# Performance work log

Hardware: AMD Instinct MI355X
Metric: run time of the kernel (lower is better)

Reference implementation:

```python
import jax, jax.numpy as jnp
import numpy as np

EMBED = 2048
NUM_EXPERTS = 64
TOP_K = 8


def setup_inputs() -> dict:
    key = jax.random.key(0)
    k1, k2, k3 = jax.random.split(key, 3)
    inputs = jax.random.normal(k1, (8, 4096, EMBED), dtype=jnp.float32)
    # nn.Linear(embed_size, num_experts): weight [num_experts, embed_size], bias [num_experts]
    W = jax.random.normal(k2, (NUM_EXPERTS, EMBED), dtype=jnp.float32) / np.sqrt(EMBED)
    b = jax.random.normal(k3, (NUM_EXPERTS,), dtype=jnp.float32) * 0.01
    return {"inputs": inputs, "W": W, "b": b}


def reference(inputs, W, b):
    # Linear projection: [B, S, E] x [E, N] -> [B, S, N]
    logits = jnp.einsum('bse,ne->bsn', inputs, W) + b
    # top-k selection along expert axis
    _, indices = jax.lax.top_k(logits, TOP_K)  # [B, S, K] int32
    # scatter mask: 1 at selected experts (one_hot sum == scatter_ of ones)
    mask = jax.nn.one_hot(indices, NUM_EXPERTS, dtype=jnp.bool_).any(axis=-2)  # [B, S, N]
    # masked_fill(-inf) + softmax -> probs only on selected experts
    masked = jnp.where(mask, logits, -jnp.inf)
    probs = jax.nn.softmax(masked, axis=-1)
    return probs, indices
```

## Files before the change

kernel.cpp:

```cpp
#include <hip/hip_runtime.h>
#include <cmath>

#define NTOK 32768
#define EMB  2048
#define NEXP 64
#define TOPK 8
#define BT   64
#define KC   64

typedef __attribute__((ext_vector_type(4))) double d4;

__global__ __launch_bounds__(256) void router_mfma(
    const float* __restrict__ X,
    const float* __restrict__ W,
    const float* __restrict__ Bv,
    float* __restrict__ out)
{
    __shared__ float xs[BT * KC];
    __shared__ float ws[NEXP * KC];

    const int tid  = threadIdx.x;
    const int lane = tid & 63;
    const int wv   = tid >> 6;
    const int t0   = blockIdx.x * BT;
    const int eL   = lane & 15;
    const int q    = lane >> 4;
    const int sw   = 4 * (eL & 7);

    d4 acc[4];
    #pragma unroll
    for (int c = 0; c < 4; ++c) {
        const double b = (double)Bv[c * 16 + eL];
        acc[c] = (d4){b, b, b, b};
    }

    for (int kc0 = 0; kc0 < EMB; kc0 += KC) {
        #pragma unroll
        for (int j = 0; j < 4; ++j) {
            const int flat = tid + j * 256;
            const int r    = flat >> 4;
            const int a    = flat & 15;
            const float4 vx = *(const float4*)&X[(size_t)(t0 + r) * EMB + kc0 + 4 * a];
            const float4 vw = *(const float4*)&W[(size_t)r * EMB + kc0 + 4 * a];
            const int col = a ^ (r & 7);
            *(float4*)&xs[r * KC + 4 * col] = vx;
            *(float4*)&ws[r * KC + 4 * col] = vw;
        }
        __syncthreads();

        #pragma unroll
        for (int k4 = 0; k4 < KC; k4 += 4) {
            const int kk = (k4 + q) ^ sw;
            const double aF = (double)xs[(wv * 16 + eL) * KC + kk];
            #pragma unroll
            for (int c = 0; c < 4; ++c) {
                const double bF = (double)ws[(c * 16 + eL) * KC + kk];
                acc[c] = __builtin_amdgcn_mfma_f64_16x16x4f64(aF, bF, acc[c], 0, 0, 0);
            }
        }
        __syncthreads();
    }

    float* probs = out;
    float* idxo  = out + (size_t)NTOK * NEXP;

    #pragma unroll
    for (int i = 0; i < 4; ++i) {
        const int T = t0 + wv * 16 + q + 4 * i;
        double v[4];
        #pragma unroll
        for (int c = 0; c < 4; ++c) v[c] = acc[c][i];

        unsigned sel = 0;
        double m0 = 0.0;
        float ssum = 0.0f;
        int myIdx = 0;
        #pragma unroll
        for (int it = 0; it < TOPK; ++it) {
            double bv = -1.0e300;
            int    be = 1 << 30;
            #pragma unroll
            for (int c = 0; c < 4; ++c)
                if (!((sel >> c) & 1) && v[c] > bv) { bv = v[c]; be = c * 16 + eL; }
            double gv = bv; int ge = be;
            #pragma unroll
            for (int off = 1; off <= 8; off <<= 1) {
                const double ov = __shfl_xor(gv, off, 64);
                const int    oe = __shfl_xor(ge, off, 64);
                if (ov > gv || (ov == gv && oe < ge)) { gv = ov; ge = oe; }
            }
            if (it == 0) m0 = gv;
            ssum += __expf((float)(gv - m0));
            if ((ge & 15) == eL) sel |= 1u << (ge >> 4);
            if (eL == it) myIdx = ge;
        }
        const float inv = 1.0f / ssum;
        #pragma unroll
        for (int c = 0; c < 4; ++c) {
            const float p = ((sel >> c) & 1) ? __expf((float)(v[c] - m0)) * inv : 0.0f;
            probs[(size_t)T * NEXP + c * 16 + eL] = p;
        }
        if (eL < TOPK) idxo[(size_t)T * TOPK + eL] = (float)myIdx;
    }
}

extern "C" void kernel_launch(void* const* d_in, const int* in_sizes, int n_in,
                              void* d_out, int out_size, void* d_ws, size_t ws_size,
                              hipStream_t stream) {
    const float* X = (const float*)d_in[0];
    const float* W = (const float*)d_in[1];
    const float* B = (const float*)d_in[2];
    router_mfma<<<NTOK / BT, 256, 0, stream>>>(X, W, B, (float*)d_out);
}
```

Baseline: 456.5 us.

## Double-buffer LDS tiles and prefetch next K-chunk into registers during MFMA

```diff
diff --git a/kernel.cpp b/kernel.cpp
--- a/kernel.cpp
+++ b/kernel.cpp
@@ -7,6 +7,7 @@
 #define TOPK 8
 #define BT   64
 #define KC   64
+#define NCH  (EMB / KC)
 
 typedef __attribute__((ext_vector_type(4))) double d4;
 
@@ -16,8 +17,8 @@
     const float* __restrict__ Bv,
     float* __restrict__ out)
 {
-    __shared__ float xs[BT * KC];
-    __shared__ float ws[NEXP * KC];
+    __shared__ float xs[2][BT * KC];
+    __shared__ float ws[2][NEXP * KC];
 
     const int tid  = threadIdx.x;
     const int lane = tid & 63;
@@ -34,30 +35,53 @@
         acc[c] = (d4){b, b, b, b};
     }
 
-    for (int kc0 = 0; kc0 < EMB; kc0 += KC) {
+    float4 rx[4], rw[4];
+
+    auto load_chunk = [&](int ch) {
+        const int kc0 = ch * KC;
         #pragma unroll
         for (int j = 0; j < 4; ++j) {
             const int flat = tid + j * 256;
             const int r    = flat >> 4;
             const int a    = flat & 15;
-            const float4 vx = *(const float4*)&X[(size_t)(t0 + r) * EMB + kc0 + 4 * a];
-            const float4 vw = *(const float4*)&W[(size_t)r * EMB + kc0 + 4 * a];
-            const int col = a ^ (r & 7);
-            *(float4*)&xs[r * KC + 4 * col] = vx;
-            *(float4*)&ws[r * KC + 4 * col] = vw;
+            rx[j] = *(const float4*)&X[(size_t)(t0 + r) * EMB + kc0 + 4 * a];
+            rw[j] = *(const float4*)&W[(size_t)r * EMB + kc0 + 4 * a];
         }
-        __syncthreads();
+    };
+    auto store_chunk = [&](int buf) {
+        #pragma unroll
+        for (int j = 0; j < 4; ++j) {
+            const int flat = tid + j * 256;
+            const int r    = flat >> 4;
+            const int a    = flat & 15;
+            const int col  = a ^ (r & 7);
+            *(float4*)&xs[buf][r * KC + 4 * col] = rx[j];
+            *(float4*)&ws[buf][r * KC + 4 * col] = rw[j];
+        }
+    };
 
+    load_chunk(0);
+    store_chunk(0);
+    __syncthreads();
+
+    for (int ch = 0; ch < NCH; ++ch) {
+        const int cur = ch & 1;
+        if (ch + 1 < NCH) load_chunk(ch + 1);
+
+        const float* xb = &xs[cur][(wv * 16 + eL) * KC];
+        const float* wb = ws[cur];
         #pragma unroll
         for (int k4 = 0; k4 < KC; k4 += 4) {
             const int kk = (k4 + q) ^ sw;
-            const double aF = (double)xs[(wv * 16 + eL) * KC + kk];
+            const double aF = (double)xb[kk];
             #pragma unroll
             for (int c = 0; c < 4; ++c) {
-                const double bF = (double)ws[(c * 16 + eL) * KC + kk];
+                const double bF = (double)wb[(c * 16 + eL) * KC + kk];
                 acc[c] = __builtin_amdgcn_mfma_f64_16x16x4f64(aF, bF, acc[c], 0, 0, 0);
             }
         }
+
+        if (ch + 1 < NCH) store_chunk((ch + 1) & 1);
         __syncthreads();
     }
 
```

Result: slower. 586.2 us (+28.4%).

## Load GEMM operands directly into registers with double-buffered prefetch, dropping LDS

Applied to the files above, without the earlier changes.

```diff
diff --git a/kernel.cpp b/kernel.cpp
--- a/kernel.cpp
+++ b/kernel.cpp
@@ -6,26 +6,28 @@
 #define NEXP 64
 #define TOPK 8
 #define BT   64
-#define KC   64
+#define KC   16
+#define NCH  (EMB / KC)
 
 typedef __attribute__((ext_vector_type(4))) double d4;
 
-__global__ __launch_bounds__(256) void router_mfma(
+__global__ __launch_bounds__(256, 4) void router_mfma(
     const float* __restrict__ X,
     const float* __restrict__ W,
     const float* __restrict__ Bv,
     float* __restrict__ out)
 {
-    __shared__ float xs[BT * KC];
-    __shared__ float ws[NEXP * KC];
-
     const int tid  = threadIdx.x;
     const int lane = tid & 63;
     const int wv   = tid >> 6;
     const int t0   = blockIdx.x * BT;
     const int eL   = lane & 15;
     const int q    = lane >> 4;
-    const int sw   = 4 * (eL & 7);
+
+    const float* xr = X + (size_t)(t0 + wv * 16 + eL) * EMB + q;
+    const float* wr[4];
+    #pragma unroll
+    for (int c = 0; c < 4; ++c) wr[c] = W + (size_t)(c * 16 + eL) * EMB + q;
 
     d4 acc[4];
     #pragma unroll
@@ -34,32 +36,42 @@
         acc[c] = (d4){b, b, b, b};
     }
 
-    for (int kc0 = 0; kc0 < EMB; kc0 += KC) {
-        #pragma unroll
-        for (int j = 0; j < 4; ++j) {
-            const int flat = tid + j * 256;
-            const int r    = flat >> 4;
-            const int a    = flat & 15;
-            const float4 vx = *(const float4*)&X[(size_t)(t0 + r) * EMB + kc0 + 4 * a];
-            const float4 vw = *(const float4*)&W[(size_t)r * EMB + kc0 + 4 * a];
-            const int col = a ^ (r & 7);
-            *(float4*)&xs[r * KC + 4 * col] = vx;
-            *(float4*)&ws[r * KC + 4 * col] = vw;
-        }
-        __syncthreads();
+    float a0[4], a1[4], b0[16], b1[16];
 
-        #pragma unroll
-        for (int k4 = 0; k4 < KC; k4 += 4) {
-            const int kk = (k4 + q) ^ sw;
-            const double aF = (double)xs[(wv * 16 + eL) * KC + kk];
-            #pragma unroll
-            for (int c = 0; c < 4; ++c) {
-                const double bF = (double)ws[(c * 16 + eL) * KC + kk];
-                acc[c] = __builtin_amdgcn_mfma_f64_16x16x4f64(aF, bF, acc[c], 0, 0, 0);
-            }
-        }
-        __syncthreads();
+#define LOADC(ch, A, B)                                        \
+    {                                                          \
+        const int kc = (ch) * KC;                              \
+        _Pragma("unroll")                                      \
+        for (int s = 0; s < 4; ++s) {                          \
+            A[s] = xr[kc + 4 * s];                             \
+            _Pragma("unroll")                                  \
+            for (int c = 0; c < 4; ++c)                        \
+                B[c * 4 + s] = wr[c][kc + 4 * s];              \
+        }                                                      \
     }
+
+#define COMPUTE(A, B)                                          \
+    {                                                          \
+        _Pragma("unroll")                                      \
+        for (int s = 0; s < 4; ++s) {                          \
+            const double aF = (double)A[s];                    \
+            _Pragma("unroll")                                  \
+            for (int c = 0; c < 4; ++c)                        \
+                acc[c] = __builtin_amdgcn_mfma_f64_16x16x4f64( \
+                    aF, (double)B[c * 4 + s], acc[c], 0, 0, 0);\
+        }                                                      \
+    }
+
+    LOADC(0, a0, b0);
+    LOADC(1, a1, b1);
+    for (int ch = 0; ch < NCH; ch += 2) {
+        COMPUTE(a0, b0);
+        if (ch + 2 < NCH) LOADC(ch + 2, a0, b0);
+        COMPUTE(a1, b1);
+        if (ch + 3 < NCH) LOADC(ch + 3, a1, b1);
+    }
+#undef LOADC
+#undef COMPUTE
 
     float* probs = out;
     float* idxo  = out + (size_t)NTOK * NEXP;
```

Result: slower. 833.6 us (+82.6%).

## Replace FP64 MFMA router GEMM with split-bf16 MFMA plus FP64 refinement of near-ties

Applied to the files above, without the earlier changes.

```diff
diff --git a/kernel.cpp b/kernel.cpp
--- a/kernel.cpp
+++ b/kernel.cpp
@@ -6,101 +6,214 @@
 #define NEXP 64
 #define TOPK 8
 #define BT   64
-#define KC   64
-
-typedef __attribute__((ext_vector_type(4))) double d4;
-
-__global__ __launch_bounds__(256) void router_mfma(
-    const float* __restrict__ X,
-    const float* __restrict__ W,
-    const float* __restrict__ Bv,
-    float* __restrict__ out)
+#define KC   32
+#define NCH  (EMB / KC)
+#define DELTA 1e-4f
+#define WL_CAP 32768
+#define WOFF  (256*1024)
+#define PLANE (NEXP*EMB)
+
+typedef __attribute__((ext_vector_type(8))) short bf8;
+typedef __attribute__((ext_vector_type(4))) float f4;
+
+__device__ __forceinline__ unsigned short bf16rn(float x){
+    union{float f; unsigned u;} c; c.f = x;
+    return (unsigned short)((c.u + 0x7FFFu + ((c.u >> 16) & 1u)) >> 16);
+}
+__device__ __forceinline__ float bf2f(unsigned short b){
+    union{unsigned u; float f;} c; c.u = ((unsigned)b) << 16; return c.f;
+}
+__device__ __forceinline__ void gld16(const void* g, void* lds){
+    __builtin_amdgcn_global_load_lds(
+        (const __attribute__((address_space(1))) void*)g,
+        (__attribute__((address_space(3))) void*)lds, 16, 0, 0);
+}
+
+__global__ __launch_bounds__(256) void wsplit(const float* __restrict__ W,
+                                              unsigned short* __restrict__ wp){
+    int i = blockIdx.x * 256 + threadIdx.x;
+    #pragma unroll
+    for (int rep = 0; rep < 2; ++rep, i += 65536){
+        const float x = W[i];
+        const unsigned short b1 = bf16rn(x);  const float r  = x - bf2f(b1);
+        const unsigned short b2 = bf16rn(r);  const float r2 = r - bf2f(b2);
+        const unsigned short b3 = bf16rn(r2);
+        wp[i] = b1; wp[PLANE + i] = b2; wp[2*PLANE + i] = b3;
+    }
+}
+
+__global__ __launch_bounds__(256) void router_bf16(
+    const float* __restrict__ X, const unsigned short* __restrict__ WP,
+    const float* __restrict__ Bv, float* __restrict__ out, int* __restrict__ wsi)
 {
-    __shared__ float xs[BT * KC];
-    __shared__ float ws[NEXP * KC];
-
-    const int tid  = threadIdx.x;
-    const int lane = tid & 63;
-    const int wv   = tid >> 6;
-    const int t0   = blockIdx.x * BT;
-    const int eL   = lane & 15;
-    const int q    = lane >> 4;
-    const int sw   = 4 * (eL & 7);
-
-    d4 acc[4];
+    __shared__ __align__(16) unsigned short xs[2][3][BT*KC];
+    __shared__ __align__(16) unsigned short wsh[2][3][NEXP*KC];
+
+    const int tid = threadIdx.x, lane = tid & 63, wv = tid >> 6;
+    const int t0 = blockIdx.x * BT;
+    const int eL = lane & 15, q = lane >> 4;
+
+    const int sr = tid >> 2, sj = tid & 3;
+    const float* xg = X + (size_t)(t0 + sr)*EMB + 8*sj;
+    const int rw = wv*16 + (lane >> 2);
+    const unsigned short* wg = WP + (size_t)rw*EMB + 8*(lane & 3);
+
+    f4 acc[4];
     #pragma unroll
-    for (int c = 0; c < 4; ++c) {
-        const double b = (double)Bv[c * 16 + eL];
-        acc[c] = (d4){b, b, b, b};
-    }
-
-    for (int kc0 = 0; kc0 < EMB; kc0 += KC) {
-        #pragma unroll
-        for (int j = 0; j < 4; ++j) {
-            const int flat = tid + j * 256;
-            const int r    = flat >> 4;
-            const int a    = flat & 15;
-            const float4 vx = *(const float4*)&X[(size_t)(t0 + r) * EMB + kc0 + 4 * a];
-            const float4 vw = *(const float4*)&W[(size_t)r * EMB + kc0 + 4 * a];
-            const int col = a ^ (r & 7);
-            *(float4*)&xs[r * KC + 4 * col] = vx;
-            *(float4*)&ws[r * KC + 4 * col] = vw;
-        }
-        __syncthreads();
-
-        #pragma unroll
-        for (int k4 = 0; k4 < KC; k4 += 4) {
-            const int kk = (k4 + q) ^ sw;
-            const double aF = (double)xs[(wv * 16 + eL) * KC + kk];
-            #pragma unroll
-            for (int c = 0; c < 4; ++c) {
-                const double bF = (double)ws[(c * 16 + eL) * KC + kk];
-                acc[c] = __builtin_amdgcn_mfma_f64_16x16x4f64(aF, bF, acc[c], 0, 0, 0);
-            }
-        }
+    for (int c = 0; c < 4; ++c){ const float b = Bv[c*16+eL]; acc[c] = (f4){b,b,b,b}; }
+
+    float xr[8];
+    auto loadX = [&](int ch){
+        const float4 v0 = *(const float4*)(xg + (size_t)ch*KC);
+        const float4 v1 = *(const float4*)(xg + (size_t)ch*KC + 4);
+        xr[0]=v0.x; xr[1]=v0.y; xr[2]=v0.z; xr[3]=v0.w;
+        xr[4]=v1.x; xr[5]=v1.y; xr[6]=v1.z; xr[7]=v1.w;
+    };
+    auto gldW = [&](int ch, int buf){
+        #pragma unroll
+        for (int s = 0; s < 3; ++s)
+            gld16(wg + (size_t)s*PLANE + ch*KC, &wsh[buf][s][wv*512]);
+    };
+    auto writeX = [&](int buf){
+        bf8 o0, o1, o2;
+        #pragma unroll
+        for (int j = 0; j < 8; ++j){
+            const float x = xr[j];
+            const unsigned short b1 = bf16rn(x);  const float r  = x - bf2f(b1);
+            const unsigned short b2 = bf16rn(r);  const float r2 = r - bf2f(b2);
+            o0[j] = (short)b1; o1[j] = (short)b2; o2[j] = (short)bf16rn(r2);
+        }
+        *(bf8*)&xs[buf][0][sr*KC + 8*sj] = o0;
+        *(bf8*)&xs[buf][1][sr*KC + 8*sj] = o1;
+        *(bf8*)&xs[buf][2][sr*KC + 8*sj] = o2;
+    };
+
+    loadX(0); gldW(0, 0); writeX(0);
+    __syncthreads();
+
+    for (int ch = 0; ch < NCH; ++ch){
+        const int buf = ch & 1;
+        if (ch + 1 < NCH){ loadX(ch+1); gldW(ch+1, buf^1); }
+
+        const int rA = (wv*16 + eL)*KC + q*8;
+        const bf8 a0 = *(const bf8*)&xs[buf][0][rA];
+        const bf8 a1 = *(const bf8*)&xs[buf][1][rA];
+        const bf8 a2 = *(const bf8*)&xs[buf][2][rA];
+        #pragma unroll
+        for (int c = 0; c < 4; ++c){
+            const int rB = (c*16 + eL)*KC + q*8;
+            const bf8 b0 = *(const bf8*)&wsh[buf][0][rB];
+            const bf8 b1 = *(const bf8*)&wsh[buf][1][rB];
+            const bf8 b2 = *(const bf8*)&wsh[buf][2][rB];
+            acc[c] = __builtin_amdgcn_mfma_f32_16x16x32_bf16(a1, b1, acc[c], 0,0,0);
+            acc[c] = __builtin_amdgcn_mfma_f32_16x16x32_bf16(a0, b2, acc[c], 0,0,0);
+            acc[c] = __builtin_amdgcn_mfma_f32_16x16x32_bf16(a2, b0, acc[c], 0,0,0);
+            acc[c] = __builtin_amdgcn_mfma_f32_16x16x32_bf16(a0, b1, acc[c], 0,0,0);
+            acc[c] = __builtin_amdgcn_mfma_f32_16x16x32_bf16(a1, b0, acc[c], 0,0,0);
+            acc[c] = __builtin_amdgcn_mfma_f32_16x16x32_bf16(a0, b0, acc[c], 0,0,0);
+        }
+        if (ch + 1 < NCH) writeX(buf^1);
         __syncthreads();
     }
 
     float* probs = out;
     float* idxo  = out + (size_t)NTOK * NEXP;
+    int* wl = wsi + 4;
 
     #pragma unroll
-    for (int i = 0; i < 4; ++i) {
-        const int T = t0 + wv * 16 + q + 4 * i;
-        double v[4];
+    for (int i = 0; i < 4; ++i){
+        const int T = t0 + wv*16 + 4*q + i;
+        float v[4];
         #pragma unroll
         for (int c = 0; c < 4; ++c) v[c] = acc[c][i];
 
-        unsigned sel = 0;
-        double m0 = 0.0;
-        float ssum = 0.0f;
+        unsigned sel = 0; float m0 = 0.0f, ssum = 0.0f, prevm = 0.0f, mingap = 1e30f;
         int myIdx = 0;
         #pragma unroll
-        for (int it = 0; it < TOPK; ++it) {
-            double bv = -1.0e300;
-            int    be = 1 << 30;
+        for (int it = 0; it < 9; ++it){
+            float bv = -1e30f; int be = 1 << 30;
             #pragma unroll
             for (int c = 0; c < 4; ++c)
-                if (!((sel >> c) & 1) && v[c] > bv) { bv = v[c]; be = c * 16 + eL; }
-            double gv = bv; int ge = be;
+                if (!((sel >> c) & 1) && v[c] > bv){ bv = v[c]; be = c*16 + eL; }
+            float gv = bv; int ge = be;
             #pragma unroll
-            for (int off = 1; off <= 8; off <<= 1) {
-                const double ov = __shfl_xor(gv, off, 64);
-                const int    oe = __shfl_xor(ge, off, 64);
-                if (ov > gv || (ov == gv && oe < ge)) { gv = ov; ge = oe; }
+            for (int off = 1; off <= 8; off <<= 1){
+                const float ov = __shfl_xor(gv, off, 64);
+                const int   oe = __shfl_xor(ge, off, 64);
+                if (ov > gv || (ov == gv && oe < ge)){ gv = ov; ge = oe; }
             }
-            if (it == 0) m0 = gv;
-            ssum += __expf((float)(gv - m0));
-            if ((ge & 15) == eL) sel |= 1u << (ge >> 4);
-            if (eL == it) myIdx = ge;
+            if (it > 0) mingap = fminf(mingap, prevm - gv);
+            prevm = gv;
+            if (it < 8){
+                if (it == 0) m0 = gv;
+                ssum += __expf(gv - m0);
+                if ((ge & 15) == eL) sel |= 1u << (ge >> 4);
+                if (eL == it) myIdx = ge;
+            }
+        }
+        if (eL == 0 && mingap < DELTA){
+            const int pos = atomicAdd(wsi, 1);
+            if (pos < WL_CAP) wl[pos] = T;
         }
         const float inv = 1.0f / ssum;
         #pragma unroll
-        for (int c = 0; c < 4; ++c) {
-            const float p = ((sel >> c) & 1) ? __expf((float)(v[c] - m0)) * inv : 0.0f;
-            probs[(size_t)T * NEXP + c * 16 + eL] = p;
+        for (int c = 0; c < 4; ++c){
+            const float p = ((sel >> c) & 1) ? __expf(v[c] - m0) * inv : 0.0f;
+            probs[(size_t)T * NEXP + c*16 + eL] = p;
         }
         if (eL < TOPK) idxo[(size_t)T * TOPK + eL] = (float)myIdx;
+    }
+}
+
+__global__ __launch_bounds__(256) void refine(
+    const float* __restrict__ X, const float* __restrict__ W,
+    const float* __restrict__ Bv, float* __restrict__ out, const int* __restrict__ wsi)
+{
+    __shared__ double part[4][64];
+    const int tid = threadIdx.x, lane = tid & 63, w = tid >> 6;
+    int n = wsi[0]; if (n > WL_CAP) n = WL_CAP;
+    const int* wl = wsi + 4;
+    float* probs = out;
+    float* idxo  = out + (size_t)NTOK * NEXP;
+
+    for (int slot = blockIdx.x; slot < n; slot += gridDim.x){
+        const int T = wl[slot];
+        const float4* xr = (const float4*)(X + (size_t)T*EMB) + w*128;
+        const float4* wr = (const float4*)(W + (size_t)lane*EMB) + w*128;
+        double a0=0, a1=0, a2=0, a3=0;
+        #pragma unroll 4
+        for (int i = 0; i < 128; ++i){
+            const float4 xv = xr[i], wv4 = wr[i];
+            a0 += (double)xv.x * (double)wv4.x;
+            a1 += (double)xv.y * (double)wv4.y;
+            a2 += (double)xv.z * (double)wv4.z;
+            a3 += (double)xv.w * (double)wv4.w;
+        }
+        part[w][lane] = (a0 + a1) + (a2 + a3);
+        __syncthreads();
+        if (w == 0){
+            const double v = (double)Bv[lane] +
+                part[0][lane] + part[1][lane] + part[2][lane] + part[3][lane];
+            bool selb = false; int myIdx = 0; double m0 = 0.0; float ssum = 0.0f;
+            #pragma unroll
+            for (int it = 0; it < TOPK; ++it){
+                double x = selb ? -1.0e300 : v;
+                double m = x;
+                #pragma unroll
+                for (int off = 32; off > 0; off >>= 1)
+                    m = fmax(m, __shfl_xor(m, off, 64));
+                const unsigned long long bm = __ballot(x == m);
+                const int src = __ffsll(bm) - 1;
+                if (lane == src) selb = true;
+                if (lane == it)  myIdx = src;
+                if (it == 0)     m0 = m;
+                ssum += __expf((float)(m - m0));
+            }
+            const float p = selb ? __expf((float)(v - m0)) / ssum : 0.0f;
+            probs[(size_t)T * NEXP + lane] = p;
+            if (lane < TOPK) idxo[(size_t)T * TOPK + lane] = (float)myIdx;
+        }
+        __syncthreads();
     }
 }
 
@@ -110,5 +223,9 @@
     const float* X = (const float*)d_in[0];
     const float* W = (const float*)d_in[1];
     const float* B = (const float*)d_in[2];
-    router_mfma<<<NTOK / BT, 256, 0, stream>>>(X, W, B, (float*)d_out);
-}
+    unsigned short* wp = (unsigned short*)((char*)d_ws + WOFF);
+    hipMemsetAsync(d_ws, 0, 16, stream);
+    wsplit<<<256, 256, 0, stream>>>(W, wp);
+    router_bf16<<<NTOK/BT, 256, 0, stream>>>(X, wp, B, (float*)d_out, (int*)d_ws);
+    refine<<<512, 256, 0, stream>>>(X, W, B, (float*)d_out, (const int*)d_ws);
+}
```

New measurement: 459.1 us. Within noise of the previous version (+0.6%).
